# Optimization experiments

Measured on AMD Instinct MI355X. Metric: run time of the kernel, lower is better.

Reference implementation:

```python
import jax, jax.numpy as jnp
import numpy as np
import math

B, T = 2, 1024
D_MODEL = 1024
N_HEAD = 16
HEAD_DIM = D_MODEL // N_HEAD
VOCAB = 32000
NUM_LOOP = 4
EPS_LN = 1e-5                       # torch LayerNorm default
EPS_RMS = float(np.finfo(np.float32).eps)  # torch RMSNorm eps=None -> finfo eps


def setup_inputs() -> dict:
    key = jax.random.key(0)
    ks = jax.random.split(key, 12)
    s = 0.02
    d = D_MODEL
    tok = jax.random.normal(ks[1], (VOCAB, d), jnp.float32) * s
    tok = tok.at[0].set(0.0)  # padding_idx=0
    return {
        "idx": jax.random.randint(ks[0], (B, T), 0, VOCAB),
        "tok_embed": tok,
        "ln_e_g": jnp.ones((d,), jnp.float32),
        "ln_e_b": jnp.zeros((d,), jnp.float32),
        "Wqkv": jax.random.normal(ks[2], (d, 3 * d), jnp.float32) * s,
        "bqkv": jnp.zeros((3 * d,), jnp.float32),
        "Wo": jax.random.normal(ks[3], (d, d), jnp.float32) * s,
        "bo": jnp.zeros((d,), jnp.float32),
        "W1": jax.random.normal(ks[4], (d, 4 * d), jnp.float32) * s,
        "b1": jnp.zeros((4 * d,), jnp.float32),
        "W2": jax.random.normal(ks[5], (4 * d, d), jnp.float32) * s,
        "b2": jnp.zeros((d,), jnp.float32),
        "n1_w": jnp.ones((d,), jnp.float32),
        "n2_w": jnp.ones((d,), jnp.float32),
        "lnf_g": jnp.ones((d,), jnp.float32),
        "lnf_b": jnp.zeros((d,), jnp.float32),
        "Wlm": jax.random.normal(ks[6], (d, VOCAB), jnp.float32) * s,
        "blm": jnp.zeros((VOCAB,), jnp.float32),
    }


def layernorm(x, g, b):
    m = jnp.mean(x, axis=-1, keepdims=True)
    v = jnp.mean(jnp.square(x - m), axis=-1, keepdims=True)
    return (x - m) * jax.lax.rsqrt(v + EPS_LN) * g + b


def rmsnorm(x, w):
    ms = jnp.mean(jnp.square(x), axis=-1, keepdims=True)
    return x * jax.lax.rsqrt(ms + EPS_RMS) * w


def gelu_tanh(x):
    c = math.sqrt(2.0 / math.pi)
    return 0.5 * x * (1.0 + jnp.tanh(c * (x + 0.044715 * x * x * x)))


def alibi_causal_bias(t):
    # rpe[q,k] = -(q-k) for q>k else 0, scaled per head by 2^(-8/H*(h+1)); causal -inf above diag
    pos = jnp.arange(t)
    rel = pos[:, None] - pos[None, :]                      # [T,T] = q - k
    slopes = 2.0 ** (-8.0 / N_HEAD * jnp.arange(1, N_HEAD + 1, dtype=jnp.float32))
    bias = -slopes[:, None, None] * rel.astype(jnp.float32)  # [H,T,T]
    return jnp.where(rel[None] >= 0, bias, -jnp.inf)       # causal mask fused


def reference(idx, tok_embed, ln_e_g, ln_e_b, Wqkv, bqkv, Wo, bo,
              W1, b1, W2, b2, n1_w, n2_w, lnf_g, lnf_b, Wlm, blm):
    b, t = idx.shape
    x = layernorm(tok_embed[idx], ln_e_g, ln_e_b)          # rpe=True: no sinusoidal PE
    bias = alibi_causal_bias(t)                            # [H,T,T]
    scale = 1.0 / math.sqrt(HEAD_DIM)

    for _ in range(NUM_LOOP):
        # attention sublayer
        h = rmsnorm(x, n1_w)
        qkv = h @ Wqkv + bqkv
        q, k, v = jnp.split(qkv, 3, axis=-1)
        q = q.reshape(b, t, N_HEAD, HEAD_DIM).transpose(0, 2, 1, 3)
        k = k.reshape(b, t, N_HEAD, HEAD_DIM).transpose(0, 2, 1, 3)
        v = v.reshape(b, t, N_HEAD, HEAD_DIM).transpose(0, 2, 1, 3)
        att = jnp.einsum('bhqd,bhkd->bhqk', q, k) * scale + bias[None]
        att = jax.nn.softmax(att, axis=-1)
        y = jnp.einsum('bhqk,bhkd->bhqd', att, v)
        y = y.transpose(0, 2, 1, 3).reshape(b, t, D_MODEL)
        x = x + (y @ Wo + bo)
        # mlp sublayer
        h = rmsnorm(x, n2_w)
        x = x + (gelu_tanh(h @ W1 + b1) @ W2 + b2)

    x = layernorm(x, lnf_g, lnf_b)
    return x @ Wlm + blm  # [B,T,VOCAB]
```

## Files before the change

### kernel.cpp

```cpp
#include <hip/hip_runtime.h>
#include <stdint.h>

#define DEVI __device__ __forceinline__

typedef __attribute__((ext_vector_type(8))) short short8;
typedef __attribute__((ext_vector_type(4))) float f32x4;
typedef unsigned short u16;
typedef unsigned int u32;

typedef const __attribute__((address_space(1))) void* gas_ptr;
typedef __attribute__((address_space(3))) void* las_ptr;

constexpr int BBATCH = 2;
constexpr int TT  = 1024;
constexpr int BT  = BBATCH * TT;
constexpr int DM  = 1024;
constexpr int NH  = 16;
constexpr int HD  = 64;
constexpr int DFF = 4096;
constexpr int NV  = 32000;
constexpr int NL  = 4;

DEVI u16 f2b(float f) {
  u32 u = __builtin_bit_cast(u32, f);
  u = (u + 0x7fffu + ((u >> 16) & 1u)) >> 16;
  return (u16)u;
}
DEVI float b2f(u16 h) { return __builtin_bit_cast(float, (u32)h << 16); }

DEVI void gld16(const void* g, void* l) {
  __builtin_amdgcn_global_load_lds((gas_ptr)g, (las_ptr)l, 16, 0, 0);
}

DEVI float wave_sum(float v) {
#pragma unroll
  for (int off = 32; off; off >>= 1) v += __shfl_xor(v, off);
  return v;
}
DEVI float block_sum(float v, float* sb) {
  v = wave_sum(v);
  int lane = threadIdx.x & 63, wid = threadIdx.x >> 6;
  __syncthreads();
  if (lane == 0) sb[wid] = v;
  __syncthreads();
  return sb[0] + sb[1] + sb[2] + sb[3];
}

DEVI float gelu_f(float x) {
  float u = 0.7978845608028654f * (x + 0.044715f * x * x * x);
  float e = __expf(2.0f * u);
  return x * (1.0f - 1.0f / (e + 1.0f));
}

__global__ __launch_bounds__(256) void wt_transpose(const float* __restrict__ in,
                                                    u16* __restrict__ out, int K, int N) {
  __shared__ float t[32][33];
  int n0 = blockIdx.x * 32, k0 = blockIdx.y * 32;
  int tx = threadIdx.x, ty = threadIdx.y;
#pragma unroll
  for (int i = 0; i < 4; ++i)
    t[ty + 8 * i][tx] = in[(size_t)(k0 + ty + 8 * i) * N + n0 + tx];
  __syncthreads();
#pragma unroll
  for (int i = 0; i < 4; ++i)
    out[(size_t)(n0 + ty + 8 * i) * K + k0 + tx] = f2b(t[tx][ty + 8 * i]);
}

__global__ __launch_bounds__(256) void v_transpose(const u16* __restrict__ qkv,
                                                   u16* __restrict__ vT) {
  __shared__ u16 t[32][33];
  int bh = blockIdx.z, b = bh >> 4, h = bh & 15;
  int d0 = blockIdx.x * 32, t0 = blockIdx.y * 32;
  int tx = threadIdx.x, ty = threadIdx.y;
  const u16* src = qkv + (size_t)b * TT * 3 * DM + 2 * DM + h * HD;
#pragma unroll
  for (int i = 0; i < 4; ++i)
    t[ty + 8 * i][tx] = src[(size_t)(t0 + ty + 8 * i) * (3 * DM) + d0 + tx];
  __syncthreads();
  u16* dst = vT + (size_t)bh * HD * TT;
#pragma unroll
  for (int i = 0; i < 4; ++i)
    dst[(size_t)(d0 + ty + 8 * i) * TT + t0 + tx] = t[tx][ty + 8 * i];
}

__global__ __launch_bounds__(256) void embed_ln_k(const int* __restrict__ idx,
                                                  const float* __restrict__ tok,
                                                  const float* __restrict__ g,
                                                  const float* __restrict__ b,
                                                  float* __restrict__ x) {
  __shared__ float sb[4];
  int row = blockIdx.x, tid = threadIdx.x;
  float4 v = ((const float4*)(tok + (size_t)idx[row] * DM))[tid];
  float s = block_sum(v.x + v.y + v.z + v.w, sb);
  float m = s * (1.0f / DM);
  float dx = v.x - m, dy = v.y - m, dz = v.z - m, dw = v.w - m;
  float q = block_sum(dx * dx + dy * dy + dz * dz + dw * dw, sb);
  float rs = rsqrtf(q * (1.0f / DM) + 1e-5f);
  float4 gg = ((const float4*)g)[tid];
  float4 bb = ((const float4*)b)[tid];
  float4 o = make_float4(dx * rs * gg.x + bb.x, dy * rs * gg.y + bb.y,
                         dz * rs * gg.z + bb.z, dw * rs * gg.w + bb.w);
  ((float4*)(x + (size_t)row * DM))[tid] = o;
}

__global__ __launch_bounds__(256) void final_ln_k(const float* __restrict__ x,
                                                  const float* __restrict__ g,
                                                  const float* __restrict__ b,
                                                  u16* __restrict__ xf) {
  __shared__ float sb[4];
  int row = blockIdx.x, tid = threadIdx.x;
  float4 v = ((const float4*)(x + (size_t)row * DM))[tid];
  float s = block_sum(v.x + v.y + v.z + v.w, sb);
  float m = s * (1.0f / DM);
  float dx = v.x - m, dy = v.y - m, dz = v.z - m, dw = v.w - m;
  float q = block_sum(dx * dx + dy * dy + dz * dz + dw * dw, sb);
  float rs = rsqrtf(q * (1.0f / DM) + 1e-5f);
  float4 gg = ((const float4*)g)[tid];
  float4 bb = ((const float4*)b)[tid];
  u32 lo = (u32)f2b(dx * rs * gg.x + bb.x) | ((u32)f2b(dy * rs * gg.y + bb.y) << 16);
  u32 hi = (u32)f2b(dz * rs * gg.z + bb.z) | ((u32)f2b(dw * rs * gg.w + bb.w) << 16);
  ((uint2*)(xf + (size_t)row * DM))[tid] = make_uint2(lo, hi);
}

__global__ __launch_bounds__(256) void rmsnorm_k(const float* __restrict__ x,
                                                 const float* __restrict__ w,
                                                 u16* __restrict__ h) {
  __shared__ float sb[4];
  int row = blockIdx.x, tid = threadIdx.x;
  float4 v = ((const float4*)(x + (size_t)row * DM))[tid];
  float q = block_sum(v.x * v.x + v.y * v.y + v.z * v.z + v.w * v.w, sb);
  float rs = rsqrtf(q * (1.0f / DM) + 1.1920928955078125e-7f);
  float4 ww = ((const float4*)w)[tid];
  u32 lo = (u32)f2b(v.x * rs * ww.x) | ((u32)f2b(v.y * rs * ww.y) << 16);
  u32 hi = (u32)f2b(v.z * rs * ww.z) | ((u32)f2b(v.w * rs * ww.w) << 16);
  ((uint2*)(h + (size_t)row * DM))[tid] = make_uint2(lo, hi);
}

__global__ __launch_bounds__(256) void attn_k(const u16* __restrict__ qkv,
                                              const u16* __restrict__ vT,
                                              u16* __restrict__ y) {
  __shared__ __align__(16) char sP[32768];
  __shared__ __align__(16) char sK[2][16384];
  __shared__ __align__(16) char sV[2][16384];
  const int tid = threadIdx.x, lane = tid & 63, wid = tid >> 6;
  const int qt = blockIdx.x, bh = blockIdx.y, b = bh >> 4, h = bh & 15;
  const float slope = exp2f(-0.5f * (float)(h + 1));

  const char* Qb = (const char*)(qkv + (size_t)b * TT * 3 * DM + h * HD);
  const char* Kb = (const char*)(qkv + (size_t)b * TT * 3 * DM + DM + h * HD);
  const char* Vb = (const char*)(vT + (size_t)bh * HD * TT);

#pragma unroll
  for (int ci = 0; ci < 4; ++ci) {
    int c = wid * 4 + ci;
    int r = c * 8 + (lane >> 3);
    int q = (lane & 7) ^ (r & 7);
    gld16(Qb + (size_t)(qt * 128 + r) * 6144 + q * 16, sP + c * 1024 + lane * 16);
  }

  auto stageKV = [&](int buf, int kt) {
    int kv0 = kt * 128;
#pragma unroll
    for (int ci = 0; ci < 4; ++ci) {
      int c = wid * 4 + ci;
      int r = c * 8 + (lane >> 3);
      int q = (lane & 7) ^ (r & 7);
      gld16(Kb + (size_t)(kv0 + r) * 6144 + q * 16, sK[buf] + c * 1024 + lane * 16);
    }
#pragma unroll
    for (int ci = 0; ci < 4; ++ci) {
      int c = wid * 4 + ci;
      int d = c * 4 + (lane >> 4);
      int q = (lane & 15) ^ (d & 15);
      gld16(Vb + (size_t)d * 2048 + (size_t)kv0 * 2 + q * 16, sV[buf] + c * 1024 + lane * 16);
    }
  };
  stageKV(0, 0);
  asm volatile("s_waitcnt vmcnt(8)" ::: "memory");

  short8 qf[2][2];
#pragma unroll
  for (int i = 0; i < 2; ++i)
#pragma unroll
    for (int ks = 0; ks < 2; ++ks) {
      int r = wid * 32 + i * 16 + (lane & 15);
      int q = ((ks << 2) + (lane >> 4)) ^ (r & 7);
      qf[i][ks] = *(const short8*)(sP + r * 128 + q * 16);
    }

  f32x4 Y[2][4] = {};
  float m_r[2][4], l_r[2][4];
#pragma unroll
  for (int i = 0; i < 2; ++i)
#pragma unroll
    for (int r = 0; r < 4; ++r) { m_r[i][r] = -3e38f; l_r[i][r] = 0.0f; }

  for (int kt = 0; kt <= qt; ++kt) {
    const int cur = kt & 1;
    if (kt < qt) {
      stageKV(cur ^ 1, kt + 1);
      asm volatile("s_waitcnt vmcnt(8)" ::: "memory");
    } else {
      asm volatile("s_waitcnt vmcnt(0)" ::: "memory");
    }
    __syncthreads();

    f32x4 s[2][8] = {};
#pragma unroll
    for (int ks = 0; ks < 2; ++ks) {
      short8 kf[8];
#pragma unroll
      for (int j = 0; j < 8; ++j) {
        int r = j * 16 + (lane & 15);
        int q = ((ks << 2) + (lane >> 4)) ^ (r & 7);
        kf[j] = *(const short8*)(sK[cur] + r * 128 + q * 16);
      }
#pragma unroll
      for (int i = 0; i < 2; ++i)
#pragma unroll
        for (int j = 0; j < 8; ++j)
          s[i][j] = __builtin_amdgcn_mfma_f32_16x16x32_bf16(qf[i][ks], kf[j], s[i][j], 0, 0, 0);
    }

    const int kv0 = kt * 128;
#pragma unroll
    for (int i = 0; i < 2; ++i) {
      const int qbase = qt * 128 + wid * 32 + i * 16 + ((lane >> 4) << 2);
      float rowmax[4] = {-3e38f, -3e38f, -3e38f, -3e38f};
#pragma unroll
      for (int j = 0; j < 8; ++j) {
        int kcol = kv0 + j * 16 + (lane & 15);
#pragma unroll
        for (int r = 0; r < 4; ++r) {
          int qrow = qbase + r;
          float v = (kcol <= qrow) ? s[i][j][r] * 0.125f - slope * (float)(qrow - kcol) : -3e38f;
          s[i][j][r] = v;
          rowmax[r] = fmaxf(rowmax[r], v);
        }
      }
#pragma unroll
      for (int r = 0; r < 4; ++r) {
        rowmax[r] = fmaxf(rowmax[r], __shfl_xor(rowmax[r], 1));
        rowmax[r] = fmaxf(rowmax[r], __shfl_xor(rowmax[r], 2));
        rowmax[r] = fmaxf(rowmax[r], __shfl_xor(rowmax[r], 4));
        rowmax[r] = fmaxf(rowmax[r], __shfl_xor(rowmax[r], 8));
        float mn = fmaxf(m_r[i][r], rowmax[r]);
        float al = __expf(m_r[i][r] - mn);
        m_r[i][r] = mn;
        l_r[i][r] *= al;
#pragma unroll
        for (int j = 0; j < 4; ++j) Y[i][j][r] *= al;
      }
      float rs[4] = {0.0f, 0.0f, 0.0f, 0.0f};
#pragma unroll
      for (int j = 0; j < 8; ++j)
#pragma unroll
        for (int r = 0; r < 4; ++r) {
          float p = __expf(s[i][j][r] - m_r[i][r]);
          s[i][j][r] = p;
          rs[r] += p;
        }
#pragma unroll
      for (int r = 0; r < 4; ++r) {
        rs[r] += __shfl_xor(rs[r], 1);
        rs[r] += __shfl_xor(rs[r], 2);
        rs[r] += __shfl_xor(rs[r], 4);
        rs[r] += __shfl_xor(rs[r], 8);
        l_r[i][r] += rs[r];
      }
#pragma unroll
      for (int j = 0; j < 8; ++j)
#pragma unroll
        for (int r = 0; r < 4; ++r) {
          int rl = wid * 32 + i * 16 + ((lane >> 4) << 2) + r;
          int c = j * 16 + (lane & 15);
          int g = c >> 3;
          *(u16*)(sP + rl * 256 + ((g ^ (rl & 15)) << 4) + (c & 7) * 2) = f2b(s[i][j][r]);
        }
    }

#pragma unroll
    for (int ks = 0; ks < 4; ++ks) {
      short8 pf[2], vf[4];
#pragma unroll
      for (int i = 0; i < 2; ++i) {
        int r = wid * 32 + i * 16 + (lane & 15);
        int q = ((ks << 2) + (lane >> 4)) ^ (r & 15);
        pf[i] = *(const short8*)(sP + r * 256 + (q << 4));
      }
#pragma unroll
      for (int j = 0; j < 4; ++j) {
        int d = j * 16 + (lane & 15);
        int q = ((ks << 2) + (lane >> 4)) ^ (d & 15);
        vf[j] = *(const short8*)(sV[cur] + d * 256 + (q << 4));
      }
#pragma unroll
      for (int i = 0; i < 2; ++i)
#pragma unroll
        for (int j = 0; j < 4; ++j)
          Y[i][j] = __builtin_amdgcn_mfma_f32_16x16x32_bf16(pf[i], vf[j], Y[i][j], 0, 0, 0);
    }
    __syncthreads();
  }

#pragma unroll
  for (int i = 0; i < 2; ++i)
#pragma unroll
    for (int r = 0; r < 4; ++r) {
      float inv = 1.0f / l_r[i][r];
      int qrow = qt * 128 + wid * 32 + i * 16 + ((lane >> 4) << 2) + r;
      u16* yp = y + (size_t)(b * TT + qrow) * DM + h * HD;
#pragma unroll
      for (int j = 0; j < 4; ++j)
        yp[j * 16 + (lane & 15)] = f2b(Y[i][j][r] * inv);
    }
}

enum { EPI_BF16 = 0, EPI_GELU = 1, EPI_ADDF32 = 2, EPI_F32 = 3 };

template <int BM, int BN, int WM, int WN, int EPI>
__global__ __launch_bounds__(256, 2) void gemm_bt(
    const u16* __restrict__ A, int lda, const u16* __restrict__ Bt, int ldb,
    const float* __restrict__ bias, void* __restrict__ C, int ldc,
    float* __restrict__ resid, int K) {
  constexpr int BK = 64;
  constexpr int NW = WM * WN;
  constexpr int FM = BM / WM / 16, FN = BN / WN / 16;
  constexpr int ABYTES = BM * BK * 2, BBYTES = BN * BK * 2;
  constexpr int ACH = ABYTES / 1024, BCH = BBYTES / 1024, NCH = ACH + BCH;
  extern __shared__ __align__(16) char smem[];

  const int tid = threadIdx.x, lane = tid & 63, wid = tid >> 6;
  const int brow = blockIdx.y * BM, bcol = blockIdx.x * BN;

  const int nt = K >> 6;
  const int widm = wid / WN, widn = wid % WN;
  const int rm0 = widm * (BM / WM), cn0 = widn * (BN / WN);

  f32x4 acc[FM][FN] = {};

  const int swq16 = (((lane & 7) ^ ((lane >> 3) & 7)) << 4);
  const int lrow8 = lane >> 3;

  auto stage = [&](int buf, int kt) {
    char* base = smem + buf * (ABYTES + BBYTES);
    const char* Ag = (const char*)A;
    const char* Bg = (const char*)Bt;
    long long kOff = (long long)kt * 128 + swq16;
#pragma unroll
    for (int ci = 0; ci < NCH / NW; ++ci) {
      int c = wid + ci * NW;
      if (c < ACH) {
        int r = c * 8 + lrow8;
        gld16(Ag + (long long)(brow + r) * (lda * 2) + kOff, base + c * 1024 + lane * 16);
      } else {
        int r = (c - ACH) * 8 + lrow8;
        gld16(Bg + (long long)(bcol + r) * (ldb * 2) + kOff,
              base + ABYTES + (c - ACH) * 1024 + lane * 16);
      }
    }
  };

  auto compute = [&](int buf) {
    char* baseA = smem + buf * (ABYTES + BBYTES);
    char* baseB = baseA + ABYTES;
#pragma unroll
    for (int ks = 0; ks < 2; ++ks) {
      short8 af[FM], bv[FN];
#pragma unroll
      for (int i = 0; i < FM; ++i) {
        int r = rm0 + i * 16 + (lane & 15);
        int cq = ((ks << 2) + (lane >> 4)) ^ (r & 7);
        af[i] = *(const short8*)(baseA + r * 128 + (cq << 4));
      }
#pragma unroll
      for (int j = 0; j < FN; ++j) {
        int r = cn0 + j * 16 + (lane & 15);
        int cq = ((ks << 2) + (lane >> 4)) ^ (r & 7);
        bv[j] = *(const short8*)(baseB + r * 128 + (cq << 4));
      }
#pragma unroll
      for (int i = 0; i < FM; ++i)
#pragma unroll
        for (int j = 0; j < FN; ++j)
          acc[i][j] = __builtin_amdgcn_mfma_f32_16x16x32_bf16(af[i], bv[j], acc[i][j], 0, 0, 0);
    }
  };

  stage(0, 0);
  __syncthreads();
  int cur = 0;
  for (int t = 0; t < nt; ++t) {
    if (t + 1 < nt) stage(cur ^ 1, t + 1);
    compute(cur);
    __syncthreads();
    cur ^= 1;
  }

  const int r0 = brow + rm0 + ((lane >> 4) << 2);
  const int c0 = bcol + cn0 + (lane & 15);
#pragma unroll
  for (int i = 0; i < FM; ++i) {
#pragma unroll
    for (int j = 0; j < FN; ++j) {
#pragma unroll
      for (int r = 0; r < 4; ++r) {
        int row = r0 + i * 16 + r;
        int col = c0 + j * 16;
        float v = acc[i][j][r];
        if constexpr (EPI == EPI_BF16) {
          ((u16*)C)[(size_t)row * ldc + col] = f2b(v + bias[col]);
        } else if constexpr (EPI == EPI_GELU) {
          ((u16*)C)[(size_t)row * ldc + col] = f2b(gelu_f(v + bias[col]));
        } else if constexpr (EPI == EPI_ADDF32) {
          size_t o = (size_t)row * ldc + col;
          resid[o] += v + bias[col];
        } else {
          ((float*)C)[(size_t)row * ldc + col] = v + bias[col];
        }
      }
    }
  }
}

template <int EPI>
__global__ __launch_bounds__(512, 2) void gemm8(
    const u16* __restrict__ A, int lda, const u16* __restrict__ Bt, int ldb,
    const float* __restrict__ bias, void* __restrict__ C, int ldc, int K, int nby) {
  __shared__ __align__(16) char smem[2][2][32768];
  const int tid = threadIdx.x, lane = tid & 63;
  const int wid = tid >> 6, wm = wid >> 2, wn = wid & 3;

  const int nb = gridDim.x;
  const int q8 = nb >> 3, r8 = nb & 7;
  const int xcd = blockIdx.x & 7, lin = blockIdx.x >> 3;
  const int idx = (xcd < r8 ? xcd * (q8 + 1) : r8 * (q8 + 1) + (xcd - r8) * q8) + lin;
  const int brow = (idx % nby) * 256, bcol = (idx / nby) * 256;

  const int nt = K >> 6, niter = nt >> 1;

  const int srow = tid >> 3, sq = tid & 7;
  auto stage = [&](int buf, int isB, int half, int kt) {
    const u16* G = isB ? Bt : A;
    const int ld = isB ? ldb : lda;
    const int base = isB ? bcol : brow;
    char* L = &smem[buf][isB][half * 16384];
#pragma unroll
    for (int l = 0; l < 2; ++l) {
      int rl = half * 128 + l * 64 + srow;
      gld16((const char*)G + (size_t)(base + rl) * (ld * 2) + kt * 128 + ((sq ^ (rl & 7)) << 4),
            L + l * 8192 + tid * 16);
    }
  };

  short8 bfr[4][2], afr[2][2];
  f32x4 acc[8][4] = {};

  stage(0, 0, 0, 0); stage(0, 0, 1, 0);
  stage(0, 1, 0, 0); stage(0, 1, 1, 0);
  stage(1, 1, 0, 1); stage(1, 1, 1, 1);
  asm volatile("s_waitcnt vmcnt(0)" ::: "memory");
  __builtin_amdgcn_s_barrier();

  for (int i = 0; i < niter; ++i) {
    const bool full = (i + 1 < niter);
    const int t2 = 2 * i + 2, t3 = 2 * i + 3;
#pragma unroll
    for (int h = 0; h < 2; ++h) {
#pragma unroll
      for (int qd = 0; qd < 4; ++qd) {
        if (qd == 0) {
#pragma unroll
          for (int j = 0; j < 4; ++j)
#pragma unroll
            for (int ks = 0; ks < 2; ++ks) {
              int r = wn * 64 + j * 16 + (lane & 15);
              int q = ((ks << 2) + (lane >> 4)) ^ (r & 7);
              bfr[j][ks] = *(const short8*)&smem[h][1][r * 128 + q * 16];
            }
        }
#pragma unroll
        for (int f = 0; f < 2; ++f)
#pragma unroll
          for (int ks = 0; ks < 2; ++ks) {
            int r = wm * 128 + (qd * 2 + f) * 16 + (lane & 15);
            int q = ((ks << 2) + (lane >> 4)) ^ (r & 7);
            afr[f][ks] = *(const short8*)&smem[h][0][r * 128 + q * 16];
          }
        if (h == 0) {
          if (qd == 0) stage(1, 0, 0, 2 * i + 1);
          else if (qd == 1) stage(1, 0, 1, 2 * i + 1);
          else if (qd == 2) { if (full) stage(0, 1, 0, t2); }
          else              { if (full) stage(0, 1, 1, t2); }
        } else {
          if (qd == 0)      { if (full) stage(0, 0, 0, t2); }
          else if (qd == 1) { if (full) stage(0, 0, 1, t2); }
          else if (qd == 2) { if (full) stage(1, 1, 0, t3); }
          else              { if (full) stage(1, 1, 1, t3); }
        }
        if (qd == 3) {
          if (full) asm volatile("s_waitcnt vmcnt(4)" ::: "memory");
          else if (h == 0) asm volatile("s_waitcnt vmcnt(0)" ::: "memory");
        }
        __builtin_amdgcn_s_barrier();
        asm volatile("s_waitcnt lgkmcnt(0)" ::: "memory");
        __builtin_amdgcn_s_setprio(1);
#pragma unroll
        for (int f = 0; f < 2; ++f)
#pragma unroll
          for (int j = 0; j < 4; ++j)
#pragma unroll
            for (int ks = 0; ks < 2; ++ks)
              acc[qd * 2 + f][j] = __builtin_amdgcn_mfma_f32_16x16x32_bf16(
                  afr[f][ks], bfr[j][ks], acc[qd * 2 + f][j], 0, 0, 0);
        __builtin_amdgcn_s_setprio(0);
        __builtin_amdgcn_s_barrier();
      }
    }
  }

  const int r0 = brow + wm * 128 + ((lane >> 4) << 2);
  const int c0 = bcol + wn * 64 + (lane & 15);
#pragma unroll
  for (int fi = 0; fi < 8; ++fi) {
#pragma unroll
    for (int j = 0; j < 4; ++j) {
      int col = c0 + j * 16;
      float bv = bias[col];
#pragma unroll
      for (int r = 0; r < 4; ++r) {
        int row = r0 + fi * 16 + r;
        float v = acc[fi][j][r] + bv;
        if constexpr (EPI == EPI_F32)
          ((float*)C)[(size_t)row * ldc + col] = v;
        else if constexpr (EPI == EPI_GELU)
          ((u16*)C)[(size_t)row * ldc + col] = f2b(gelu_f(v));
        else
          ((u16*)C)[(size_t)row * ldc + col] = f2b(v);
      }
    }
  }
}

extern "C" void kernel_launch(void* const* d_in, const int* in_sizes, int n_in,
                              void* d_out, int out_size, void* d_ws, size_t ws_size,
                              hipStream_t stream) {
  (void)in_sizes; (void)n_in; (void)out_size;
  const int*   idx    = (const int*)d_in[0];
  const float* tok    = (const float*)d_in[1];
  const float* ln_e_g = (const float*)d_in[2];
  const float* ln_e_b = (const float*)d_in[3];
  const float* Wqkv   = (const float*)d_in[4];
  const float* bqkv   = (const float*)d_in[5];
  const float* Wo     = (const float*)d_in[6];
  const float* bo     = (const float*)d_in[7];
  const float* W1     = (const float*)d_in[8];
  const float* b1     = (const float*)d_in[9];
  const float* W2     = (const float*)d_in[10];
  const float* b2     = (const float*)d_in[11];
  const float* n1_w   = (const float*)d_in[12];
  const float* n2_w   = (const float*)d_in[13];
  const float* lnf_g  = (const float*)d_in[14];
  const float* lnf_b  = (const float*)d_in[15];
  const float* Wlm    = (const float*)d_in[16];
  const float* blm    = (const float*)d_in[17];
  float* out = (float*)d_out;

  char* w = (char*)d_ws;
  auto alloc = [&](size_t bytes) { char* p = w; w += (bytes + 255) & ~(size_t)255; return p; };
  float* x   = (float*)alloc((size_t)BT * DM * 4);
  u16* h     = (u16*)alloc((size_t)BT * DM * 2);
  u16* qkv   = (u16*)alloc((size_t)BT * 3 * DM * 2);
  u16* vT    = (u16*)alloc((size_t)BBATCH * NH * HD * TT * 2);
  u16* y     = (u16*)alloc((size_t)BT * DM * 2);
  u16* act   = (u16*)alloc((size_t)BT * DFF * 2);
  u16* xf    = (u16*)alloc((size_t)BT * DM * 2);
  u16* WqkvT = (u16*)alloc((size_t)3 * DM * DM * 2);
  u16* WoT   = (u16*)alloc((size_t)DM * DM * 2);
  u16* W1T   = (u16*)alloc((size_t)DFF * DM * 2);
  u16* W2T   = (u16*)alloc((size_t)DM * DFF * 2);
  u16* WlmT  = (u16*)alloc((size_t)NV * DM * 2);
  if ((size_t)(w - (char*)d_ws) > ws_size) return;

  dim3 t328(32, 8);
  wt_transpose<<<dim3(3 * DM / 32, DM / 32), t328, 0, stream>>>(Wqkv, WqkvT, DM, 3 * DM);
  wt_transpose<<<dim3(DM / 32, DM / 32), t328, 0, stream>>>(Wo, WoT, DM, DM);
  wt_transpose<<<dim3(DFF / 32, DM / 32), t328, 0, stream>>>(W1, W1T, DM, DFF);
  wt_transpose<<<dim3(DM / 32, DFF / 32), t328, 0, stream>>>(W2, W2T, DFF, DM);
  wt_transpose<<<dim3(NV / 32, DM / 32), t328, 0, stream>>>(Wlm, WlmT, DM, NV);

  embed_ln_k<<<BT, 256, 0, stream>>>(idx, tok, ln_e_g, ln_e_b, x);

  constexpr int SM128 = 2 * (128 * 64 * 2 + 128 * 64 * 2);

  for (int l = 0; l < NL; ++l) {
    rmsnorm_k<<<BT, 256, 0, stream>>>(x, n1_w, h);
    gemm_bt<128, 128, 2, 2, EPI_BF16><<<dim3(3 * DM / 128, BT / 128), 256, SM128, stream>>>(
        h, DM, WqkvT, DM, bqkv, qkv, 3 * DM, nullptr, DM);
    v_transpose<<<dim3(HD / 32, TT / 32, BBATCH * NH), t328, 0, stream>>>(qkv, vT);
    attn_k<<<dim3(TT / 128, BBATCH * NH), 256, 0, stream>>>(qkv, vT, y);
    gemm_bt<128, 128, 2, 2, EPI_ADDF32><<<dim3(DM / 128, BT / 128), 256, SM128, stream>>>(
        y, DM, WoT, DM, bo, nullptr, DM, x, DM);
    rmsnorm_k<<<BT, 256, 0, stream>>>(x, n2_w, h);
    gemm_bt<128, 128, 2, 2, EPI_GELU><<<dim3(DFF / 128, BT / 128), 256, SM128, stream>>>(
        h, DM, W1T, DM, b1, act, DFF, nullptr, DM);
    gemm_bt<128, 128, 2, 2, EPI_ADDF32><<<dim3(DM / 128, BT / 128), 256, SM128, stream>>>(
        act, DFF, W2T, DFF, b2, nullptr, DM, x, DFF);
  }

  final_ln_k<<<BT, 256, 0, stream>>>(x, lnf_g, lnf_b, xf);
  gemm8<EPI_F32><<<dim3((NV / 256) * (BT / 256)), 512, 0, stream>>>(
      xf, DM, WlmT, DM, blm, out, NV, DM, BT / 256);
}
```

Baseline: 974.4 us.

## Merge weight transposes, prefetch A fragments, interleave epilogue stores, prioritise attention MFMAs

Replaces five weight-transpose launches with one flattened launch that picks the matrix from the block index. In the 256x256 GEMM it double-buffers A fragments so LDS reads for the next quarter overlap the current MFMAs, waiting on a partial lgkmcnt instead of a full drain. It also writes each quarter of the output during the final iteration so stores overlap the remaining math, and it raises wave priority around the attention MFMA blocks. These target launch overhead and LDS and store latency, at the cost of more live registers in the GEMM.

```diff
diff --git a/kernel.cpp b/kernel.cpp
--- a/kernel.cpp
+++ b/kernel.cpp
@@ -52,11 +52,23 @@
   return x * (1.0f - 1.0f / (e + 1.0f));
 }
 
-__global__ __launch_bounds__(256) void wt_transpose(const float* __restrict__ in,
-                                                    u16* __restrict__ out, int K, int N) {
+__global__ __launch_bounds__(256) void wt_transpose_all(
+    const float* __restrict__ Wqkv, const float* __restrict__ Wo,
+    const float* __restrict__ W1, const float* __restrict__ W2,
+    const float* __restrict__ Wlm,
+    u16* __restrict__ WqkvT, u16* __restrict__ WoT, u16* __restrict__ W1T,
+    u16* __restrict__ W2T, u16* __restrict__ WlmT) {
   __shared__ float t[32][33];
-  int n0 = blockIdx.x * 32, k0 = blockIdx.y * 32;
-  int tx = threadIdx.x, ty = threadIdx.y;
+  int bid = blockIdx.x;
+  const float* in; u16* out; int K, N, tt;
+  if (bid < 3072)       { in = Wqkv; out = WqkvT; K = 1024; N = 3072;  tt = bid; }
+  else if (bid < 4096)  { in = Wo;   out = WoT;   K = 1024; N = 1024;  tt = bid - 3072; }
+  else if (bid < 8192)  { in = W1;   out = W1T;   K = 1024; N = 4096;  tt = bid - 4096; }
+  else if (bid < 12288) { in = W2;   out = W2T;   K = 4096; N = 1024;  tt = bid - 8192; }
+  else                  { in = Wlm;  out = WlmT;  K = 1024; N = 32000; tt = bid - 12288; }
+  int nx = N >> 5;
+  int n0 = (tt % nx) * 32, k0 = (tt / nx) * 32;
+  int tx = threadIdx.x & 31, ty = threadIdx.x >> 5;
 #pragma unroll
   for (int i = 0; i < 4; ++i)
     t[ty + 8 * i][tx] = in[(size_t)(k0 + ty + 8 * i) * N + n0 + tx];
@@ -206,6 +218,7 @@
     __syncthreads();
 
     f32x4 s[2][8] = {};
+    __builtin_amdgcn_s_setprio(1);
 #pragma unroll
     for (int ks = 0; ks < 2; ++ks) {
       short8 kf[8];
@@ -221,6 +234,7 @@
         for (int j = 0; j < 8; ++j)
           s[i][j] = __builtin_amdgcn_mfma_f32_16x16x32_bf16(qf[i][ks], kf[j], s[i][j], 0, 0, 0);
     }
+    __builtin_amdgcn_s_setprio(0);
 
     const int kv0 = kt * 128;
 #pragma unroll
@@ -279,6 +293,7 @@
         }
     }
 
+    __builtin_amdgcn_s_setprio(1);
 #pragma unroll
     for (int ks = 0; ks < 4; ++ks) {
       short8 pf[2], vf[4];
@@ -300,6 +315,7 @@
         for (int j = 0; j < 4; ++j)
           Y[i][j] = __builtin_amdgcn_mfma_f32_16x16x32_bf16(pf[i], vf[j], Y[i][j], 0, 0, 0);
     }
+    __builtin_amdgcn_s_setprio(0);
     __syncthreads();
   }
 
@@ -453,8 +469,66 @@
     }
   };
 
-  short8 bfr[4][2], afr[2][2];
+  short8 bfr[4][2], afr0[2][2], afr1[2][2];
   f32x4 acc[8][4] = {};
+
+  const int r0 = brow + wm * 128 + ((lane >> 4) << 2);
+  const int c0 = bcol + wn * 64 + (lane & 15);
+  float bias_r[4];
+#pragma unroll
+  for (int j = 0; j < 4; ++j) bias_r[j] = bias[c0 + j * 16];
+
+  auto LDB = [&](int h) {
+#pragma unroll
+    for (int j = 0; j < 4; ++j)
+#pragma unroll
+      for (int ks = 0; ks < 2; ++ks) {
+        int r = wn * 64 + j * 16 + (lane & 15);
+        int q = ((ks << 2) + (lane >> 4)) ^ (r & 7);
+        bfr[j][ks] = *(const short8*)&smem[h][1][r * 128 + q * 16];
+      }
+  };
+  auto LDA = [&](short8 (&dst)[2][2], int h, int rp) {
+#pragma unroll
+    for (int f = 0; f < 2; ++f)
+#pragma unroll
+      for (int ks = 0; ks < 2; ++ks) {
+        int r = wm * 128 + (rp * 2 + f) * 16 + (lane & 15);
+        int q = ((ks << 2) + (lane >> 4)) ^ (r & 7);
+        dst[f][ks] = *(const short8*)&smem[h][0][r * 128 + q * 16];
+      }
+  };
+  auto MMA = [&](int qd, const short8 (&a)[2][2]) {
+#pragma unroll
+    for (int f = 0; f < 2; ++f)
+#pragma unroll
+      for (int j = 0; j < 4; ++j)
+#pragma unroll
+        for (int ks = 0; ks < 2; ++ks)
+          acc[qd * 2 + f][j] = __builtin_amdgcn_mfma_f32_16x16x32_bf16(
+              a[f][ks], bfr[j][ks], acc[qd * 2 + f][j], 0, 0, 0);
+  };
+  auto STQ = [&](int qd) {
+#pragma unroll
+    for (int f = 0; f < 2; ++f) {
+      int fi = qd * 2 + f;
+#pragma unroll
+      for (int j = 0; j < 4; ++j) {
+        int col = c0 + j * 16;
+#pragma unroll
+        for (int r = 0; r < 4; ++r) {
+          int row = r0 + fi * 16 + r;
+          float v = acc[fi][j][r] + bias_r[j];
+          if constexpr (EPI == EPI_F32)
+            ((float*)C)[(size_t)row * ldc + col] = v;
+          else if constexpr (EPI == EPI_GELU)
+            ((u16*)C)[(size_t)row * ldc + col] = f2b(gelu_f(v));
+          else
+            ((u16*)C)[(size_t)row * ldc + col] = f2b(v);
+        }
+      }
+    }
+  };
 
   stage(0, 0, 0, 0); stage(0, 0, 1, 0);
   stage(0, 1, 0, 0); stage(0, 1, 1, 0);
@@ -469,24 +543,9 @@
     for (int h = 0; h < 2; ++h) {
 #pragma unroll
       for (int qd = 0; qd < 4; ++qd) {
-        if (qd == 0) {
-#pragma unroll
-          for (int j = 0; j < 4; ++j)
-#pragma unroll
-            for (int ks = 0; ks < 2; ++ks) {
-              int r = wn * 64 + j * 16 + (lane & 15);
-              int q = ((ks << 2) + (lane >> 4)) ^ (r & 7);
-              bfr[j][ks] = *(const short8*)&smem[h][1][r * 128 + q * 16];
-            }
-        }
-#pragma unroll
-        for (int f = 0; f < 2; ++f)
-#pragma unroll
-          for (int ks = 0; ks < 2; ++ks) {
-            int r = wm * 128 + (qd * 2 + f) * 16 + (lane & 15);
-            int q = ((ks << 2) + (lane >> 4)) ^ (r & 7);
-            afr[f][ks] = *(const short8*)&smem[h][0][r * 128 + q * 16];
-          }
+        if (qd == 0) { LDB(h); LDA(afr0, h, 0); LDA(afr1, h, 1); }
+        else if (qd == 1) LDA(afr0, h, 2);
+        else if (qd == 2) LDA(afr1, h, 3);
         if (h == 0) {
           if (qd == 0) stage(1, 0, 0, 2 * i + 1);
           else if (qd == 1) stage(1, 0, 1, 2 * i + 1);
@@ -503,40 +562,13 @@
           else if (h == 0) asm volatile("s_waitcnt vmcnt(0)" ::: "memory");
         }
         __builtin_amdgcn_s_barrier();
-        asm volatile("s_waitcnt lgkmcnt(0)" ::: "memory");
+        if (qd < 3) asm volatile("s_waitcnt lgkmcnt(4)" ::: "memory");
+        else        asm volatile("s_waitcnt lgkmcnt(0)" ::: "memory");
         __builtin_amdgcn_s_setprio(1);
-#pragma unroll
-        for (int f = 0; f < 2; ++f)
-#pragma unroll
-          for (int j = 0; j < 4; ++j)
-#pragma unroll
-            for (int ks = 0; ks < 2; ++ks)
-              acc[qd * 2 + f][j] = __builtin_amdgcn_mfma_f32_16x16x32_bf16(
-                  afr[f][ks], bfr[j][ks], acc[qd * 2 + f][j], 0, 0, 0);
+        if (qd & 1) MMA(qd, afr1); else MMA(qd, afr0);
         __builtin_amdgcn_s_setprio(0);
+        if (!full && h == 1) STQ(qd);
         __builtin_amdgcn_s_barrier();
-      }
-    }
-  }
-
-  const int r0 = brow + wm * 128 + ((lane >> 4) << 2);
-  const int c0 = bcol + wn * 64 + (lane & 15);
-#pragma unroll
-  for (int fi = 0; fi < 8; ++fi) {
-#pragma unroll
-    for (int j = 0; j < 4; ++j) {
-      int col = c0 + j * 16;
-      float bv = bias[col];
-#pragma unroll
-      for (int r = 0; r < 4; ++r) {
-        int row = r0 + fi * 16 + r;
-        float v = acc[fi][j][r] + bv;
-        if constexpr (EPI == EPI_F32)
-          ((float*)C)[(size_t)row * ldc + col] = v;
-        else if constexpr (EPI == EPI_GELU)
-          ((u16*)C)[(size_t)row * ldc + col] = f2b(gelu_f(v));
-        else
-          ((u16*)C)[(size_t)row * ldc + col] = f2b(v);
       }
     }
   }
@@ -582,16 +614,13 @@
   u16* WlmT  = (u16*)alloc((size_t)NV * DM * 2);
   if ((size_t)(w - (char*)d_ws) > ws_size) return;
 
+  wt_transpose_all<<<44288, 256, 0, stream>>>(Wqkv, Wo, W1, W2, Wlm,
+                                              WqkvT, WoT, W1T, W2T, WlmT);
+
+  embed_ln_k<<<BT, 256, 0, stream>>>(idx, tok, ln_e_g, ln_e_b, x);
+
+  constexpr int SM128 = 2 * (128 * 64 * 2 + 128 * 64 * 2);
   dim3 t328(32, 8);
-  wt_transpose<<<dim3(3 * DM / 32, DM / 32), t328, 0, stream>>>(Wqkv, WqkvT, DM, 3 * DM);
-  wt_transpose<<<dim3(DM / 32, DM / 32), t328, 0, stream>>>(Wo, WoT, DM, DM);
-  wt_transpose<<<dim3(DFF / 32, DM / 32), t328, 0, stream>>>(W1, W1T, DM, DFF);
-  wt_transpose<<<dim3(DM / 32, DFF / 32), t328, 0, stream>>>(W2, W2T, DFF, DM);
-  wt_transpose<<<dim3(NV / 32, DM / 32), t328, 0, stream>>>(Wlm, WlmT, DM, NV);
-
-  embed_ln_k<<<BT, 256, 0, stream>>>(idx, tok, ln_e_g, ln_e_b, x);
-
-  constexpr int SM128 = 2 * (128 * 64 * 2 + 128 * 64 * 2);
 
   for (int l = 0; l < NL; ++l) {
     rmsnorm_k<<<BT, 256, 0, stream>>>(x, n1_w, h);
```

New measurement: 1.134 ms. 1.16x slower.
